# Performance work log

Measured on AMD Instinct MI355X. Metric: run time of the kernel, lower is better.

Reference implementation:

```python
import math
import jax
import jax.numpy as jnp
import numpy as np

B = 64          # graphs per batch
NPG = 1000      # nodes per graph
IN = 64         # input feature dim
H = 128         # hidden dim
DEG = 16        # avg degree
C = 10          # num classes
RATIO = 0.8     # topk ratio
EPS = 1e-5      # batchnorm eps
E = B * NPG * DEG


def setup_inputs() -> dict:
    key = jax.random.key(0)
    ks = jax.random.split(key, 16)
    x = jax.random.normal(ks[0], (B * NPG, IN), jnp.float32)
    # per-graph random edges, then offset to global node ids
    src = jax.random.randint(ks[1], (B, NPG * DEG), 0, NPG)
    dst = jax.random.randint(ks[2], (B, NPG * DEG), 0, NPG)
    off = (jnp.arange(B) * NPG)[:, None]
    edge_index = jnp.stack([(src + off).reshape(-1), (dst + off).reshape(-1)]).astype(jnp.int32)
    batch = jnp.repeat(jnp.arange(B), NPG).astype(jnp.int32)
    edge_weight = jax.random.uniform(ks[3], (E,), jnp.float32)
    # parameters: block 1 conv is [IN,H]; blocks 2-6 are [H,H] (stacked)
    conv1_w = jax.random.normal(ks[4], (IN, H), jnp.float32) * 0.05
    conv_w = jax.random.normal(ks[5], (5, H, H), jnp.float32) * 0.05
    conv_b = jnp.zeros((6, H), jnp.float32)
    bn_gamma = jnp.ones((6, H), jnp.float32)
    bn_beta = jnp.zeros((6, H), jnp.float32)
    bn_mean = jax.random.normal(ks[6], (6, H), jnp.float32) * 0.01
    bn_var = jax.random.uniform(ks[7], (6, H), jnp.float32, 0.5, 1.5)
    pool_w = jax.random.normal(ks[8], (6, H), jnp.float32)
    d1_w = jax.random.normal(ks[9], (2 * H, 4 * H), jnp.float32) * 0.05
    d1_b = jnp.zeros((4 * H,), jnp.float32)
    d2_w = jax.random.normal(ks[10], (4 * H, C), jnp.float32) * 0.05
    d2_b = jnp.zeros((C,), jnp.float32)
    return dict(x=x, edge_index=edge_index, batch=batch, edge_weight=edge_weight,
                conv1_w=conv1_w, conv_w=conv_w, conv_b=conv_b,
                bn_gamma=bn_gamma, bn_beta=bn_beta, bn_mean=bn_mean, bn_var=bn_var,
                pool_w=pool_w, d1_w=d1_w, d1_b=d1_b, d2_w=d2_w, d2_b=d2_b)


def _gcn_conv(h, src, dst, w_e, W, b, n_nodes):
    # PyG GCNConv: add self-loops (weight 1), sym-normalize, aggregate at dst
    xw = h @ W                                        # [N, H]
    deg = jnp.zeros((n_nodes,), h.dtype).at[dst].add(w_e) + 1.0
    dinv = jax.lax.rsqrt(deg)
    coef = dinv[src] * dinv[dst] * w_e                # [E]
    out = jnp.zeros_like(xw).at[dst].add(coef[:, None] * xw[src])
    out = out + (dinv * dinv)[:, None] * xw + b       # self-loop term + bias
    return out


def reference(x, edge_index, batch, edge_weight, conv1_w, conv_w, conv_b,
              bn_gamma, bn_beta, bn_mean, bn_var, pool_w, d1_w, d1_b, d2_w, d2_b):
    src, dst = edge_index[0], edge_index[1]
    w_e = edge_weight
    h = x
    n_cur = NPG
    flats = jnp.zeros((B, 2 * H), x.dtype)
    for i in range(6):
        N = B * n_cur
        W = conv1_w if i == 0 else conv_w[i - 1]
        hc = _gcn_conv(h, src, dst, w_e, W, conv_b[i], N)
        # BatchNorm (inference) + ReLU
        hc = (hc - bn_mean[i]) * (bn_gamma[i] * jax.lax.rsqrt(bn_var[i] + EPS)) + bn_beta[i]
        hc = jax.nn.relu(hc)
        # TopKPooling: score = tanh(x.w/||w||), keep top ceil(ratio*n) per graph
        pw = pool_w[i]
        score = jnp.tanh(hc @ pw / jnp.linalg.norm(pw))   # [N]
        k = math.ceil(RATIO * n_cur)
        vals, idx = jax.lax.top_k(score.reshape(B, n_cur), k)  # [B,k]
        perm = (idx + (jnp.arange(B) * n_cur)[:, None]).reshape(-1)
        h = hc[perm] * vals.reshape(-1, 1)                # [B*k, H]
        # remap/filter edges; dead edges become (0,0) with weight 0
        inv = jnp.full((N,), -1, jnp.int32).at[perm].set(jnp.arange(B * k, dtype=jnp.int32))
        ok = (inv[src] >= 0) & (inv[dst] >= 0)
        src = jnp.where(ok, inv[src], 0)
        dst = jnp.where(ok, inv[dst], 0)
        w_e = jnp.where(ok, w_e, 0.0)
        n_cur = k
        hb = h.reshape(B, k, H)
        flats = flats + jnp.concatenate([hb.mean(axis=1), hb.max(axis=1)], axis=-1)
    # MLP head (dropout is identity in eval)
    hd = jax.nn.relu(flats @ d1_w + d1_b)
    return hd @ d2_w + d2_b
```

## Files before the change

kernel.cpp:

```cpp
#include <hip/hip_runtime.h>
#include <float.h>
#include <math.h>

#define NGR 64
#define NPG0 1000
#define HDIM 128
#define EG 16000
#define NE (NGR*EG)
#define RPS 1008
#define BNEPS 1e-5f
#define POOL_NB 16

typedef short short8 __attribute__((ext_vector_type(8)));
typedef float f4v __attribute__((ext_vector_type(4)));

__global__ __launch_bounds__(256) void k_wsplit(const float* __restrict__ c1w,
    const float* __restrict__ cw, const float* __restrict__ pw,
    unsigned short* __restrict__ wh, unsigned short* __restrict__ wl,
    float* __restrict__ invnorm){
  int l = blockIdx.x, t = threadIdx.x;
  __shared__ float red[2];
  if(t < 128){
    float v = pw[l*HDIM + t];
    float s = v*v;
    #pragma unroll
    for(int o=32;o>0;o>>=1) s += __shfl_down(s, o, 64);
    if((t & 63)==0) red[t>>6] = s;
  }
  __syncthreads();
  if(t==0) invnorm[l] = 1.0f / sqrtf(red[0]+red[1]);
  int K  = (l==0) ? 64 : 128;
  int sh = (l==0) ? 6 : 7;
  const float* src = (l==0) ? c1w : (cw + (size_t)(l-1)*16384);
  int tot = 128*K;
  for(int o=t;o<tot;o+=256){
    int c = o >> sh, k = o & (K-1);
    float f = src[k*128 + c];
    unsigned u  = __float_as_uint(f);
    unsigned uh = (u + 0x7fffu + ((u>>16)&1u)) & 0xffff0000u;
    float r = f - __uint_as_float(uh);
    unsigned v = __float_as_uint(r);
    int o2 = (k>>3)*1024 + c*8 + (k&7);
    wh[(size_t)l*16384 + o2] = (unsigned short)(uh>>16);
    wl[(size_t)l*16384 + o2] = (unsigned short)((v + 0x7fffu + ((v>>16)&1u))>>16);
  }
}

__global__ __launch_bounds__(256) void k_count0(const int* __restrict__ dst,
    const float* __restrict__ we, int* __restrict__ pcnt, float* __restrict__ pdeg){
  int g = blockIdx.x >> 2, sub = blockIdx.x & 3, t = threadIdx.x;
  __shared__ int   cnt[NPG0];
  __shared__ float degl[NPG0];
  for(int i=t;i<NPG0;i+=256){ cnt[i]=0; degl[i]=0.f; }
  __syncthreads();
  int base = g*EG + sub*4000;
  for(int idx=t; idx<4000; idx+=256){
    int e = base + idx;
    int ld = dst[e] - g*NPG0;
    atomicAdd(&cnt[ld], 1);
    atomicAdd(&degl[ld], we[e]);
  }
  __syncthreads();
  int p = blockIdx.x * NPG0;
  for(int i=t;i<NPG0;i+=256){ pcnt[p+i] = cnt[i]; pdeg[p+i] = degl[i]; }
}

__global__ __launch_bounds__(1024) void k_build(const int* __restrict__ pcnt,
    const float* __restrict__ pdeg, const int* __restrict__ src,
    const int* __restrict__ dst, const float* __restrict__ we,
    int* __restrict__ rp, float* __restrict__ dinvz, float* __restrict__ gsc,
    long long* __restrict__ ec){
  int g = blockIdx.x, t = threadIdx.x;
  __shared__ int sc[2][1024];
  __shared__ int cur[NPG0];
  int c = 0;
  if(t < NPG0){
    c = pcnt[(g*4+0)*NPG0+t] + pcnt[(g*4+1)*NPG0+t]
      + pcnt[(g*4+2)*NPG0+t] + pcnt[(g*4+3)*NPG0+t];
    float dg = pdeg[(g*4+0)*NPG0+t] + pdeg[(g*4+1)*NPG0+t]
             + pdeg[(g*4+2)*NPG0+t] + pdeg[(g*4+3)*NPG0+t];
    float dv = 1.0f / sqrtf(dg + 1.0f);
    dinvz[g*NPG0+t] = dv;
    gsc[g*NPG0+t]   = dv;
  }
  sc[0][t] = c;
  __syncthreads();
  int buf = 0;
  for(int d=1; d<1024; d<<=1){
    int v = sc[buf][t];
    if(t>=d) v += sc[buf][t-d];
    sc[buf^1][t] = v;
    __syncthreads();
    buf ^= 1;
  }
  if(t<=NPG0) rp[g*RPS+t] = (t==0) ? 0 : sc[buf][t-1];
  if(t<NPG0)  cur[t]      = (t==0) ? 0 : sc[buf][t-1];
  __syncthreads();
  int base = g*EG;
  for(int idx=t; idx<EG; idx+=1024){
    int e = base + idx;
    int ld = dst[e] - g*NPG0;
    int pos = atomicAdd(&cur[ld], 1);
    ec[(size_t)base + pos] = (((long long)__float_as_int(we[e]))<<32) | (unsigned)src[e];
  }
}

template<int L0>
__global__ __launch_bounds__(256) void k_agg(int n, const int* __restrict__ nlist,
    const int* __restrict__ rp, const long long* __restrict__ ec,
    const float* __restrict__ dinvz, const float* __restrict__ gsc,
    const float* __restrict__ h, float* __restrict__ agg){
  int g = blockIdx.x & 63;
  int chunk = blockIdx.x >> 6;
  int wid = threadIdx.x >> 6, lane = threadIdx.x & 63;
  const int wpg = (gridDim.x >> 6) * 4;
  const int qw   = lane >> 4, sl16 = lane & 15;
  for(int j = chunk*4 + wid; j < n; j += wpg){
    int cg = g*n + j;
    int d  = L0 ? (g*NPG0 + j) : nlist[cg];
    int ld = d - g*NPG0;
    int e0 = rp[g*RPS+ld], e1 = rp[g*RPS+ld+1];
    float dvd = dinvz[d];
    float gsd = gsc[d];
    float4 a0; a0.x=0.f; a0.y=0.f; a0.z=0.f; a0.w=0.f;
    float4 a1; a1.x=0.f; a1.y=0.f; a1.z=0.f; a1.w=0.f;
    for(int b=e0;b<e1;b+=64){
      int mm = e1-b; if(mm>64) mm=64;
      long long rec = (lane<mm) ? ec[(size_t)g*EG + b + lane] : 0;
      int   sl = (int)(rec & 0xffffffffLL);
      float cl = __int_as_float((int)(rec>>32)) * gsc[sl];
      long long pk = (((long long)__float_as_int(cl))<<32) | (unsigned)sl;
      int mr = (mm+15) & ~15;
      for(int jj=0;jj<mr;jj+=16){
        #pragma unroll
        for(int u=0;u<4;u++){
          long long p = __shfl(pk, jj + 4*u + qw, 64);
          float c = __int_as_float((int)(p>>32));
          if(c != 0.f){
            int s = (int)(p & 0xffffffffLL);
            if(L0){
              float4 hv = *(const float4*)(h + (size_t)s*64 + 4*sl16);
              a0.x += c*hv.x; a0.y += c*hv.y; a0.z += c*hv.z; a0.w += c*hv.w;
            } else {
              const float4* hp = (const float4*)(h + (size_t)s*HDIM + 8*sl16);
              float4 h0 = hp[0], h1 = hp[1];
              a0.x += c*h0.x; a0.y += c*h0.y; a0.z += c*h0.z; a0.w += c*h0.w;
              a1.x += c*h1.x; a1.y += c*h1.y; a1.z += c*h1.z; a1.w += c*h1.w;
            }
          }
        }
      }
    }
    a0.x += __shfl_xor(a0.x, 16, 64); a0.y += __shfl_xor(a0.y, 16, 64);
    a0.z += __shfl_xor(a0.z, 16, 64); a0.w += __shfl_xor(a0.w, 16, 64);
    a0.x += __shfl_xor(a0.x, 32, 64); a0.y += __shfl_xor(a0.y, 32, 64);
    a0.z += __shfl_xor(a0.z, 32, 64); a0.w += __shfl_xor(a0.w, 32, 64);
    if(!L0){
      a1.x += __shfl_xor(a1.x, 16, 64); a1.y += __shfl_xor(a1.y, 16, 64);
      a1.z += __shfl_xor(a1.z, 16, 64); a1.w += __shfl_xor(a1.w, 16, 64);
      a1.x += __shfl_xor(a1.x, 32, 64); a1.y += __shfl_xor(a1.y, 32, 64);
      a1.z += __shfl_xor(a1.z, 32, 64); a1.w += __shfl_xor(a1.w, 32, 64);
    }
    if(qw==0){
      if(L0){
        float4 hs = *(const float4*)(h + (size_t)d*64 + 4*sl16);
        float4 o;
        o.x = dvd*(a0.x + gsd*hs.x); o.y = dvd*(a0.y + gsd*hs.y);
        o.z = dvd*(a0.z + gsd*hs.z); o.w = dvd*(a0.w + gsd*hs.w);
        *(float4*)(agg + (size_t)cg*64 + 4*sl16) = o;
      } else {
        const float4* hp = (const float4*)(h + (size_t)d*HDIM + 8*sl16);
        float4 s0 = hp[0], s1 = hp[1];
        float4 o0, o1;
        o0.x = dvd*(a0.x + gsd*s0.x); o0.y = dvd*(a0.y + gsd*s0.y);
        o0.z = dvd*(a0.z + gsd*s0.z); o0.w = dvd*(a0.w + gsd*s0.w);
        o1.x = dvd*(a1.x + gsd*s1.x); o1.y = dvd*(a1.y + gsd*s1.y);
        o1.z = dvd*(a1.z + gsd*s1.z); o1.w = dvd*(a1.w + gsd*s1.w);
        float4* op = (float4*)(agg + (size_t)cg*HDIM + 8*sl16);
        op[0] = o0; op[1] = o1;
      }
    }
  }
}

__device__ inline void bfsplit(float f, unsigned short &h, unsigned short &l){
  unsigned u  = __float_as_uint(f);
  unsigned uh = (u + 0x7fffu + ((u>>16)&1u)) & 0xffff0000u;
  float r = f - __uint_as_float(uh);
  unsigned v = __float_as_uint(r);
  h = (unsigned short)(uh>>16);
  l = (unsigned short)((v + 0x7fffu + ((v>>16)&1u))>>16);
}

template<int KIN>
__global__ __launch_bounds__(256) void k_gemm_mfma(const float* __restrict__ Ain,
    const unsigned short* __restrict__ Wh, const unsigned short* __restrict__ Wl,
    const float* __restrict__ bias, const float* __restrict__ gamma,
    const float* __restrict__ beta, const float* __restrict__ mean,
    const float* __restrict__ var, const float* __restrict__ pw,
    const float* __restrict__ invn_p, const int* __restrict__ olist,
    float* __restrict__ hout, float* __restrict__ score){
  __shared__ __attribute__((aligned(16))) unsigned short AsH[64*KIN];
  __shared__ __attribute__((aligned(16))) unsigned short AsL[64*KIN];
  __shared__ float sp[64][2];
  int t = threadIdx.x;
  int r0 = blockIdx.x * 64;
  const int lane = t & 63, wid = t >> 6;
  const int wr = wid >> 1, wc = wid & 1;
  const int lr = lane & 15, lq = lane >> 4;

  constexpr int ACH = KIN/4;
  constexpr int ANP = 64*ACH/256;
  #pragma unroll
  for(int p=0;p<ANP;p++){
    int idx = p*256 + t;
    int row = idx / ACH, cq = idx % ACH;
    float4 a = *(const float4*)(Ain + (size_t)(r0+row)*KIN + cq*4);
    ushort4 h4, l4;
    bfsplit(a.x, h4.x, l4.x); bfsplit(a.y, h4.y, l4.y);
    bfsplit(a.z, h4.z, l4.z); bfsplit(a.w, h4.w, l4.w);
    int off = (row*(KIN*2) + cq*8) ^ ((row&7)<<4);
    *(ushort4*)((char*)AsH + off) = h4;
    *(ushort4*)((char*)AsL + off) = l4;
  }
  __syncthreads();

  f4v acc[2][4];
  #pragma unroll
  for(int m=0;m<2;m++)
    #pragma unroll
    for(int n=0;n<4;n++){ acc[m][n][0]=0.f; acc[m][n][1]=0.f; acc[m][n][2]=0.f; acc[m][n][3]=0.f; }

  #pragma unroll
  for(int ks=0; ks<KIN/32; ks++){
    short8 ah[2], al[2], bh[4], bl[4];
    int kb = ks*64 + lq*16;
    int panel = ks*4 + lq;
    #pragma unroll
    for(int n=0;n<4;n++){
      int col = wc*64 + n*16 + lr;
      int goff = (panel*128 + col)*8;
      bh[n] = *(const short8*)(Wh + goff);
      bl[n] = *(const short8*)(Wl + goff);
    }
    #pragma unroll
    for(int m=0;m<2;m++){
      int row = wr*32 + m*16 + lr;
      int off = (row*(KIN*2) + kb) ^ ((row&7)<<4);
      ah[m] = *(const short8*)((const char*)AsH + off);
      al[m] = *(const short8*)((const char*)AsL + off);
    }
    #pragma unroll
    for(int m=0;m<2;m++){
      #pragma unroll
      for(int n=0;n<4;n++){
        acc[m][n] = __builtin_amdgcn_mfma_f32_16x16x32_bf16(ah[m], bh[n], acc[m][n], 0,0,0);
        acc[m][n] = __builtin_amdgcn_mfma_f32_16x16x32_bf16(ah[m], bl[n], acc[m][n], 0,0,0);
        acc[m][n] = __builtin_amdgcn_mfma_f32_16x16x32_bf16(al[m], bh[n], acc[m][n], 0,0,0);
        acc[m][n] = __builtin_amdgcn_mfma_f32_16x16x32_bf16(al[m], bl[n], acc[m][n], 0,0,0);
      }
    }
  }

  float invn = invn_p[0];
  float bi[4], scv[4], bt[4], mn[4], pv[4];
  #pragma unroll
  for(int n=0;n<4;n++){
    int c = wc*64 + n*16 + lr;
    bi[n]  = bias[c];
    scv[n] = gamma[c] * (1.0f/sqrtf(var[c] + BNEPS));
    bt[n]  = beta[c];
    mn[n]  = mean[c];
    pv[n]  = pw[c];
  }
  #pragma unroll
  for(int m=0;m<2;m++){
    #pragma unroll
    for(int i=0;i<4;i++){
      int rl  = wr*32 + m*16 + lq*4 + i;
      int row = r0 + rl;
      int orig = olist ? olist[row] : row;
      float p = 0.f;
      #pragma unroll
      for(int n=0;n<4;n++){
        float v = fmaxf((acc[m][n][i] + bi[n] - mn[n])*scv[n] + bt[n], 0.f);
        hout[(size_t)orig*HDIM + wc*64 + n*16 + lr] = v;
        p += v*pv[n];
      }
      p += __shfl_xor(p, 1, 64); p += __shfl_xor(p, 2, 64);
      p += __shfl_xor(p, 4, 64); p += __shfl_xor(p, 8, 64);
      if(lr==0) sp[rl][wc] = p;
    }
  }
  __syncthreads();
  if(t < 64) score[r0 + t] = tanhf((sp[t][0] + sp[t][1]) * invn);
}

__global__ __launch_bounds__(512) void k_topk(int n, int k,
    const float* __restrict__ score, const int* __restrict__ curlist,
    float* __restrict__ vals, int* __restrict__ nextlist,
    float* __restrict__ dinvz, float* __restrict__ gsc){
  int g = blockIdx.x, t = threadIdx.x;
  __shared__ unsigned keys[1024];
  __shared__ int hist[256];
  __shared__ int ssum[256];
  __shared__ int sc2[2][512];
  __shared__ int eqbuf[1024];
  __shared__ int eqn;
  __shared__ int sh_B, sh_need, sh_E, sh_cut;
  __shared__ unsigned sh_pref;
  for(int i=t;i<n;i+=512){
    unsigned b = __float_as_uint(score[g*n+i]);
    keys[i] = (b & 0x80000000u) ? ~b : (b | 0x80000000u);
  }
  if(t==0){ sh_need = k; sh_pref = 0u; sh_cut = 0x7fffffff; }
  __syncthreads();
  for(int pass=0; pass<4; pass++){
    int shift = 24 - 8*pass;
    if(t<256) hist[t]=0;
    __syncthreads();
    unsigned pref = sh_pref; int need = sh_need;
    for(int i=t;i<n;i+=512){
      unsigned u = keys[i];
      bool m = (pass==0) || ((u >> (shift+8)) == pref);
      if(m) atomicAdd(&hist[(u>>shift)&255], 1);
    }
    __syncthreads();
    if(t<256) ssum[t] = hist[t];
    __syncthreads();
    for(int d=1; d<256; d<<=1){
      int v=0;
      if(t<256) v = ssum[t] + ((t+d<256)? ssum[t+d] : 0);
      __syncthreads();
      if(t<256) ssum[t] = v;
      __syncthreads();
    }
    if(t<256){
      int Sgt = ssum[t] - hist[t];
      if(Sgt < need && need <= ssum[t]) sh_B = t;
    }
    __syncthreads();
    int B = sh_B;
    if(t==0){
      sh_need = need - (ssum[B] - hist[B]);
      sh_pref = (pass==0) ? (unsigned)B : ((pref<<8) | (unsigned)B);
      if(pass==3) sh_E = hist[B];
    }
    __syncthreads();
  }
  unsigned T = sh_pref; int r_eq = sh_need; int E = sh_E;
  if(E > r_eq){
    if(t==0) eqn = 0;
    __syncthreads();
    for(int i=t;i<n;i+=512) if(keys[i]==T){ int p=atomicAdd(&eqn,1); eqbuf[p]=i; }
    __syncthreads();
    if(t==0){
      int last = -1;
      for(int j=0;j<r_eq;j++){
        int mn = 0x7fffffff;
        for(int q=0;q<E;q++){ int v=eqbuf[q]; if(v>last && v<mn) mn=v; }
        last = mn;
      }
      sh_cut = last;
    }
    __syncthreads();
  }
  int cut = sh_cut;
  int c0=0, c1=0;
  {
    int i=t;
    if(i<n){ unsigned u=keys[i]; c0 = (u>T) || (u==T && i<=cut); }
    i=t+512;
    if(i<n){ unsigned u=keys[i]; c1 = (u>T) || (u==T && i<=cut); }
  }
  sc2[0][t] = c0+c1;
  __syncthreads();
  int buf=0;
  for(int d=1; d<512; d<<=1){
    int v = sc2[buf][t];
    if(t>=d) v += sc2[buf][t-d];
    sc2[buf^1][t]=v;
    __syncthreads();
    buf^=1;
  }
  int base = (t==0) ? 0 : sc2[buf][t-1];
  {
    int i=t;
    if(i<n){
      int orig = curlist ? curlist[g*n+i] : (g*NPG0 + i);
      if(c0){
        unsigned u=keys[i];
        float f = __uint_as_float((u & 0x80000000u) ? (u ^ 0x80000000u) : ~u);
        vals[g*k+base]=f; nextlist[g*k+base]=orig; base++;
      } else { dinvz[orig]=0.f; gsc[orig]=0.f; }
    }
    i=t+512;
    if(i<n){
      int orig = curlist ? curlist[g*n+i] : (g*NPG0 + i);
      if(c1){
        unsigned u=keys[i];
        float f = __uint_as_float((u & 0x80000000u) ? (u ^ 0x80000000u) : ~u);
        vals[g*k+base]=f; nextlist[g*k+base]=orig;
      } else { dinvz[orig]=0.f; gsc[orig]=0.f; }
    }
  }
}

__global__ __launch_bounds__(256) void k_gpd(int k, int do_deg,
    const float* __restrict__ hraw, const float* __restrict__ vals,
    const int* __restrict__ nextlist,
    float* __restrict__ sumst, float* __restrict__ maxst,
    const int* __restrict__ rp, const long long* __restrict__ ec,
    float* __restrict__ dinvz, float* __restrict__ gsc){
  int g = blockIdx.x & 63;
  int chunk = blockIdx.x >> 6;
  int wid = threadIdx.x >> 6, lane = threadIdx.x & 63;
  int ww = chunk*4 + wid;
  const int half = lane >> 5, sl32 = lane & 31;
  const int qw   = lane >> 4, sl16 = lane & 15;
  const int NH = POOL_NB*4*2;
  float4 psum; psum.x=0.f; psum.y=0.f; psum.z=0.f; psum.w=0.f;
  float4 pmax; pmax.x=-FLT_MAX; pmax.y=-FLT_MAX; pmax.z=-FLT_MAX; pmax.w=-FLT_MAX;
  for(int j = ww*2 + half; j < k; j += NH){
    float v = vals[g*k+j];
    int d = nextlist[g*k+j];
    float4 hv = *(const float4*)(hraw + (size_t)d*HDIM + 4*sl32);
    float4 o; o.x=hv.x*v; o.y=hv.y*v; o.z=hv.z*v; o.w=hv.w*v;
    psum.x+=o.x; psum.y+=o.y; psum.z+=o.z; psum.w+=o.w;
    pmax.x=fmaxf(pmax.x,o.x); pmax.y=fmaxf(pmax.y,o.y);
    pmax.z=fmaxf(pmax.z,o.z); pmax.w=fmaxf(pmax.w,o.w);
  }
  if(do_deg){
    const int NQ = POOL_NB*4*4;
    for(int j = ww*4 + qw; j < k; j += NQ){
      int d  = nextlist[g*k + j];
      int ld = d - g*NPG0;
      int e0 = rp[g*RPS+ld], e1 = rp[g*RPS+ld+1];
      float deg = 0.f;
      for(int b=e0+sl16; b<e1; b+=16){
        long long rec = ec[(size_t)g*EG + b];
        int s = (int)(rec & 0xffffffffLL);
        float w = __int_as_float((int)(rec>>32));
        if(dinvz[s] != 0.f) deg += w;
      }
      #pragma unroll
      for(int o=8;o>0;o>>=1) deg += __shfl_xor(deg, o, 64);
      if(sl16==0){
        float dv = 1.0f / sqrtf(deg + 1.0f);
        dinvz[d] = dv;
        gsc[d] = dv * vals[g*k+j];
      }
    }
  }
  psum.x += __shfl_xor(psum.x, 32, 64); psum.y += __shfl_xor(psum.y, 32, 64);
  psum.z += __shfl_xor(psum.z, 32, 64); psum.w += __shfl_xor(psum.w, 32, 64);
  pmax.x = fmaxf(pmax.x, __shfl_xor(pmax.x, 32, 64));
  pmax.y = fmaxf(pmax.y, __shfl_xor(pmax.y, 32, 64));
  pmax.z = fmaxf(pmax.z, __shfl_xor(pmax.z, 32, 64));
  pmax.w = fmaxf(pmax.w, __shfl_xor(pmax.w, 32, 64));
  __shared__ float ss[4][128];
  __shared__ float sm[4][128];
  if(half==0){
    *(float4*)&ss[wid][4*sl32] = psum;
    *(float4*)&sm[wid][4*sl32] = pmax;
  }
  __syncthreads();
  int t = threadIdx.x;
  if(t < 128){
    float s = (ss[0][t]+ss[1][t]) + (ss[2][t]+ss[3][t]);
    float m = fmaxf(fmaxf(sm[0][t], sm[1][t]), fmaxf(sm[2][t], sm[3][t]));
    sumst[(size_t)(chunk*NGR + g)*HDIM + t] = s;
    maxst[(size_t)(chunk*NGR + g)*HDIM + t] = m;
  }
}

__global__ __launch_bounds__(512) void k_head(const float* __restrict__ sumstage,
    const float* __restrict__ maxstage,
    const float* __restrict__ d1w, const float* __restrict__ d1b,
    const float* __restrict__ d2w, const float* __restrict__ d2b, float* __restrict__ out){
  const float kinv[6] = {1.f/800.f, 1.f/640.f, 1.f/512.f, 1.f/410.f, 1.f/328.f, 1.f/263.f};
  int g = blockIdx.x, j = threadIdx.x;
  __shared__ float fl[256];
  __shared__ float hd[512];
  if(j < 128){
    float s = 0.f;
    #pragma unroll
    for(int l=0;l<6;l++){
      float ls = 0.f;
      for(int c=0;c<POOL_NB;c++)
        ls += sumstage[(size_t)((l*POOL_NB + c)*NGR + g)*HDIM + j];
      s += ls * kinv[l];
    }
    fl[j] = s;
  } else if(j < 256){
    int f = j - 128;
    float m = 0.f;
    #pragma unroll
    for(int l=0;l<6;l++){
      float lm = -FLT_MAX;
      for(int c=0;c<POOL_NB;c++)
        lm = fmaxf(lm, maxstage[(size_t)((l*POOL_NB + c)*NGR + g)*HDIM + f]);
      m += lm;
    }
    fl[j] = m;
  }
  __syncthreads();
  float acc = d1b[j];
  for(int i=0;i<256;i++) acc += fl[i]*d1w[i*512+j];
  hd[j] = fmaxf(acc, 0.f);
  __syncthreads();
  if(j < 10){
    float a = d2b[j];
    for(int i=0;i<512;i++) a += hd[i]*d2w[i*10+j];
    out[g*10+j] = a;
  }
}

extern "C" void kernel_launch(void* const* d_in, const int* in_sizes, int n_in,
                              void* d_out, int out_size, void* d_ws, size_t ws_size,
                              hipStream_t stream) {
  const float* x    = (const float*)d_in[0];
  const int* ei     = (const int*)d_in[1];
  const float* ew   = (const float*)d_in[3];
  const float* conv1w = (const float*)d_in[4];
  const float* convw  = (const float*)d_in[5];
  const float* convb  = (const float*)d_in[6];
  const float* bng    = (const float*)d_in[7];
  const float* bnb    = (const float*)d_in[8];
  const float* bnm    = (const float*)d_in[9];
  const float* bnv    = (const float*)d_in[10];
  const float* poolw  = (const float*)d_in[11];
  const float* d1w    = (const float*)d_in[12];
  const float* d1b    = (const float*)d_in[13];
  const float* d2w    = (const float*)d_in[14];
  const float* d2b    = (const float*)d_in[15];
  float* out = (float*)d_out;

  char* w = (char*)d_ws;
  float* horig = (float*)w; w += (size_t)64000*128*4;
  float* hc    = (float*)w; w += (size_t)64000*128*4;
  float* agg0  = (float*)w; w += (size_t)64000*64*4;
  long long* ec = (long long*)w; w += (size_t)NE*8;
  int*   rp    = (int*)w;   w += (size_t)NGR*RPS*4;
  int*   pcnt  = (int*)w;   w += (size_t)256*NPG0*4;
  float* pdeg  = (float*)w; w += (size_t)256*NPG0*4;
  float* dinvz = (float*)w; w += (size_t)64000*4;
  float* gsc   = (float*)w; w += (size_t)64000*4;
  float* score = (float*)w; w += (size_t)64000*4;
  float* vals  = (float*)w; w += (size_t)51200*4;
  int*   listA = (int*)w;   w += (size_t)51200*4;
  int*   listB = (int*)w;   w += (size_t)51200*4;
  float* invno = (float*)w; w += 64;
  float* sumstage = (float*)w; w += (size_t)6*POOL_NB*NGR*HDIM*4;
  float* maxstage = (float*)w; w += (size_t)6*POOL_NB*NGR*HDIM*4;
  unsigned short* whi = (unsigned short*)w; w += (size_t)6*16384*2;
  unsigned short* wlo = (unsigned short*)w; w += (size_t)6*16384*2;

  k_wsplit<<<6,256,0,stream>>>(conv1w, convw, poolw, whi, wlo, invno);

  const int ns[6]={1000,800,640,512,410,328};
  const int ks[6]={800,640,512,410,328,263};

  k_count0<<<256,256,0,stream>>>(ei+NE, ew, pcnt, pdeg);
  k_build<<<64,1024,0,stream>>>(pcnt, pdeg, ei, ei+NE, ew, rp, dinvz, gsc, ec);

  k_agg<1><<<64*32,256,0,stream>>>(1000, nullptr, rp, ec, dinvz, gsc, x, agg0);
  k_gemm_mfma<64><<<1000,256,0,stream>>>(agg0, whi, wlo, convb, bng, bnb, bnm, bnv,
                                         poolw, invno, nullptr, horig, score);
  k_topk<<<64,512,0,stream>>>(1000, 800, score, nullptr, vals, listA, dinvz, gsc);
  k_gpd<<<64*POOL_NB,256,0,stream>>>(800, 1, horig, vals, listA,
                                     sumstage, maxstage, rp, ec, dinvz, gsc);

  int* cur = listA; int* nxt = listB;
  for(int i=1;i<6;i++){
    int n = ns[i], k = ks[i];
    k_agg<0><<<64*32,256,0,stream>>>(n, cur, rp, ec, dinvz, gsc, horig, hc);
    k_gemm_mfma<128><<<n,256,0,stream>>>(hc, whi + (size_t)i*16384, wlo + (size_t)i*16384,
                                         convb+i*128, bng+i*128, bnb+i*128, bnm+i*128,
                                         bnv+i*128, poolw+i*128, invno+i,
                                         cur, horig, score);
    k_topk<<<64,512,0,stream>>>(n, k, score, cur, vals, nxt, dinvz, gsc);
    k_gpd<<<64*POOL_NB,256,0,stream>>>(k, (i<5)?1:0, horig, vals, nxt,
                                       sumstage + (size_t)i*POOL_NB*NGR*HDIM,
                                       maxstage + (size_t)i*POOL_NB*NGR*HDIM,
                                       rp, ec, dinvz, gsc);
    int* tmp = cur; cur = nxt; nxt = tmp;
  }

  k_head<<<64,512,0,stream>>>(sumstage, maxstage, d1w, d1b, d2w, d2b, out);
}
```

Baseline: 484.4 us.

## Fuse neighbor aggregation into MFMA GEMM kernel via shared-memory tiles

Merges the per-layer aggregation kernel and the split-bf16 MFMA GEMM into one kernel. Each 256-thread block aggregates 32 rows (8 per wave) straight into swizzled hi/lo bf16 shared-memory tiles, then runs the GEMM, BN, ReLU and score epilogue. This drops the global round trip of the aggregated features and one launch per layer. Because the kernel now reads old h while writing new rows by original index, it ping-pongs between two h buffers. The cost is a smaller GEMM tile (32 rows, one m-fragment per wave) with less weight reuse, and a different aggregation parallel layout.

```diff
diff --git a/kernel.cpp b/kernel.cpp
--- a/kernel.cpp
+++ b/kernel.cpp
@@ -105,19 +105,41 @@
   }
 }
 
-template<int L0>
-__global__ __launch_bounds__(256) void k_agg(int n, const int* __restrict__ nlist,
+__device__ inline void bfsplit(float f, unsigned short &h, unsigned short &l){
+  unsigned u  = __float_as_uint(f);
+  unsigned uh = (u + 0x7fffu + ((u>>16)&1u)) & 0xffff0000u;
+  float r = f - __uint_as_float(uh);
+  unsigned v = __float_as_uint(r);
+  h = (unsigned short)(uh>>16);
+  l = (unsigned short)((v + 0x7fffu + ((v>>16)&1u))>>16);
+}
+
+template<int KIN>
+__global__ __launch_bounds__(256) void k_fused(const int* __restrict__ olist,
     const int* __restrict__ rp, const long long* __restrict__ ec,
     const float* __restrict__ dinvz, const float* __restrict__ gsc,
-    const float* __restrict__ h, float* __restrict__ agg){
-  int g = blockIdx.x & 63;
-  int chunk = blockIdx.x >> 6;
-  int wid = threadIdx.x >> 6, lane = threadIdx.x & 63;
-  const int wpg = (gridDim.x >> 6) * 4;
-  const int qw   = lane >> 4, sl16 = lane & 15;
-  for(int j = chunk*4 + wid; j < n; j += wpg){
-    int cg = g*n + j;
-    int d  = L0 ? (g*NPG0 + j) : nlist[cg];
+    const float* __restrict__ h,
+    const unsigned short* __restrict__ Wh, const unsigned short* __restrict__ Wl,
+    const float* __restrict__ bias, const float* __restrict__ gamma,
+    const float* __restrict__ beta, const float* __restrict__ mean,
+    const float* __restrict__ var, const float* __restrict__ pw,
+    const float* __restrict__ invn_p, float* __restrict__ hout,
+    float* __restrict__ score){
+  constexpr int L0 = (KIN==64);
+  __shared__ __attribute__((aligned(16))) unsigned short AsH[32*KIN];
+  __shared__ __attribute__((aligned(16))) unsigned short AsL[32*KIN];
+  __shared__ float sp[32][2];
+  int t = threadIdx.x;
+  int r0 = blockIdx.x * 32;
+  const int lane = t & 63, wid = t >> 6;
+  const int wr = wid >> 1, wc = wid & 1;
+  const int qw = lane >> 4, sl16 = lane & 15;
+
+  for(int rr=0; rr<8; rr++){
+    int local = wid*8 + rr;
+    int row = r0 + local;
+    int d = L0 ? row : olist[row];
+    int g = d / NPG0;
     int ld = d - g*NPG0;
     int e0 = rp[g*RPS+ld], e1 = rp[g*RPS+ld+1];
     float dvd = dinvz[d];
@@ -167,7 +189,12 @@
         float4 o;
         o.x = dvd*(a0.x + gsd*hs.x); o.y = dvd*(a0.y + gsd*hs.y);
         o.z = dvd*(a0.z + gsd*hs.z); o.w = dvd*(a0.w + gsd*hs.w);
-        *(float4*)(agg + (size_t)cg*64 + 4*sl16) = o;
+        ushort4 h4, l4;
+        bfsplit(o.x, h4.x, l4.x); bfsplit(o.y, h4.y, l4.y);
+        bfsplit(o.z, h4.z, l4.z); bfsplit(o.w, h4.w, l4.w);
+        int off = (local*128 + sl16*8) ^ ((local&7)<<4);
+        *(ushort4*)((char*)AsH + off) = h4;
+        *(ushort4*)((char*)AsL + off) = l4;
       } else {
         const float4* hp = (const float4*)(h + (size_t)d*HDIM + 8*sl16);
         float4 s0 = hp[0], s1 = hp[1];
@@ -176,89 +203,48 @@
         o0.z = dvd*(a0.z + gsd*s0.z); o0.w = dvd*(a0.w + gsd*s0.w);
         o1.x = dvd*(a1.x + gsd*s1.x); o1.y = dvd*(a1.y + gsd*s1.y);
         o1.z = dvd*(a1.z + gsd*s1.z); o1.w = dvd*(a1.w + gsd*s1.w);
-        float4* op = (float4*)(agg + (size_t)cg*HDIM + 8*sl16);
-        op[0] = o0; op[1] = o1;
+        ushort4 h4, l4;
+        int off = (local*256 + sl16*16) ^ ((local&7)<<4);
+        bfsplit(o0.x, h4.x, l4.x); bfsplit(o0.y, h4.y, l4.y);
+        bfsplit(o0.z, h4.z, l4.z); bfsplit(o0.w, h4.w, l4.w);
+        *(ushort4*)((char*)AsH + off) = h4;
+        *(ushort4*)((char*)AsL + off) = l4;
+        bfsplit(o1.x, h4.x, l4.x); bfsplit(o1.y, h4.y, l4.y);
+        bfsplit(o1.z, h4.z, l4.z); bfsplit(o1.w, h4.w, l4.w);
+        *(ushort4*)((char*)AsH + off + 8) = h4;
+        *(ushort4*)((char*)AsL + off + 8) = l4;
       }
     }
   }
-}
-
-__device__ inline void bfsplit(float f, unsigned short &h, unsigned short &l){
-  unsigned u  = __float_as_uint(f);
-  unsigned uh = (u + 0x7fffu + ((u>>16)&1u)) & 0xffff0000u;
-  float r = f - __uint_as_float(uh);
-  unsigned v = __float_as_uint(r);
-  h = (unsigned short)(uh>>16);
-  l = (unsigned short)((v + 0x7fffu + ((v>>16)&1u))>>16);
-}
-
-template<int KIN>
-__global__ __launch_bounds__(256) void k_gemm_mfma(const float* __restrict__ Ain,
-    const unsigned short* __restrict__ Wh, const unsigned short* __restrict__ Wl,
-    const float* __restrict__ bias, const float* __restrict__ gamma,
-    const float* __restrict__ beta, const float* __restrict__ mean,
-    const float* __restrict__ var, const float* __restrict__ pw,
-    const float* __restrict__ invn_p, const int* __restrict__ olist,
-    float* __restrict__ hout, float* __restrict__ score){
-  __shared__ __attribute__((aligned(16))) unsigned short AsH[64*KIN];
-  __shared__ __attribute__((aligned(16))) unsigned short AsL[64*KIN];
-  __shared__ float sp[64][2];
-  int t = threadIdx.x;
-  int r0 = blockIdx.x * 64;
-  const int lane = t & 63, wid = t >> 6;
-  const int wr = wid >> 1, wc = wid & 1;
-  const int lr = lane & 15, lq = lane >> 4;
-
-  constexpr int ACH = KIN/4;
-  constexpr int ANP = 64*ACH/256;
+  __syncthreads();
+
+  f4v acc[4];
   #pragma unroll
-  for(int p=0;p<ANP;p++){
-    int idx = p*256 + t;
-    int row = idx / ACH, cq = idx % ACH;
-    float4 a = *(const float4*)(Ain + (size_t)(r0+row)*KIN + cq*4);
-    ushort4 h4, l4;
-    bfsplit(a.x, h4.x, l4.x); bfsplit(a.y, h4.y, l4.y);
-    bfsplit(a.z, h4.z, l4.z); bfsplit(a.w, h4.w, l4.w);
-    int off = (row*(KIN*2) + cq*8) ^ ((row&7)<<4);
-    *(ushort4*)((char*)AsH + off) = h4;
-    *(ushort4*)((char*)AsL + off) = l4;
-  }
-  __syncthreads();
-
-  f4v acc[2][4];
-  #pragma unroll
-  for(int m=0;m<2;m++)
-    #pragma unroll
-    for(int n=0;n<4;n++){ acc[m][n][0]=0.f; acc[m][n][1]=0.f; acc[m][n][2]=0.f; acc[m][n][3]=0.f; }
-
+  for(int n=0;n<4;n++){ acc[n][0]=0.f; acc[n][1]=0.f; acc[n][2]=0.f; acc[n][3]=0.f; }
   #pragma unroll
   for(int ks=0; ks<KIN/32; ks++){
-    short8 ah[2], al[2], bh[4], bl[4];
-    int kb = ks*64 + lq*16;
-    int panel = ks*4 + lq;
+    short8 ah, al, bh[4], bl[4];
+    int kb = ks*64 + qw*16;
+    int panel = ks*4 + qw;
     #pragma unroll
     for(int n=0;n<4;n++){
-      int col = wc*64 + n*16 + lr;
+      int col = wc*64 + n*16 + sl16;
       int goff = (panel*128 + col)*8;
       bh[n] = *(const short8*)(Wh + goff);
       bl[n] = *(const short8*)(Wl + goff);
     }
+    {
+      int row = wr*16 + sl16;
+      int off = (row*(KIN*2) + kb) ^ ((row&7)<<4);
+      ah = *(const short8*)((const char*)AsH + off);
+      al = *(const short8*)((const char*)AsL + off);
+    }
     #pragma unroll
-    for(int m=0;m<2;m++){
-      int row = wr*32 + m*16 + lr;
-      int off = (row*(KIN*2) + kb) ^ ((row&7)<<4);
-      ah[m] = *(const short8*)((const char*)AsH + off);
-      al[m] = *(const short8*)((const char*)AsL + off);
-    }
-    #pragma unroll
-    for(int m=0;m<2;m++){
-      #pragma unroll
-      for(int n=0;n<4;n++){
-        acc[m][n] = __builtin_amdgcn_mfma_f32_16x16x32_bf16(ah[m], bh[n], acc[m][n], 0,0,0);
-        acc[m][n] = __builtin_amdgcn_mfma_f32_16x16x32_bf16(ah[m], bl[n], acc[m][n], 0,0,0);
-        acc[m][n] = __builtin_amdgcn_mfma_f32_16x16x32_bf16(al[m], bh[n], acc[m][n], 0,0,0);
-        acc[m][n] = __builtin_amdgcn_mfma_f32_16x16x32_bf16(al[m], bl[n], acc[m][n], 0,0,0);
-      }
+    for(int n=0;n<4;n++){
+      acc[n] = __builtin_amdgcn_mfma_f32_16x16x32_bf16(ah, bh[n], acc[n], 0,0,0);
+      acc[n] = __builtin_amdgcn_mfma_f32_16x16x32_bf16(ah, bl[n], acc[n], 0,0,0);
+      acc[n] = __builtin_amdgcn_mfma_f32_16x16x32_bf16(al, bh[n], acc[n], 0,0,0);
+      acc[n] = __builtin_amdgcn_mfma_f32_16x16x32_bf16(al, bl[n], acc[n], 0,0,0);
     }
   }
 
@@ -266,7 +252,7 @@
   float bi[4], scv[4], bt[4], mn[4], pv[4];
   #pragma unroll
   for(int n=0;n<4;n++){
-    int c = wc*64 + n*16 + lr;
+    int c = wc*64 + n*16 + sl16;
     bi[n]  = bias[c];
     scv[n] = gamma[c] * (1.0f/sqrtf(var[c] + BNEPS));
     bt[n]  = beta[c];
@@ -274,26 +260,23 @@
     pv[n]  = pw[c];
   }
   #pragma unroll
-  for(int m=0;m<2;m++){
+  for(int i=0;i<4;i++){
+    int rl  = wr*16 + qw*4 + i;
+    int row = r0 + rl;
+    int orig = olist ? olist[row] : row;
+    float p = 0.f;
     #pragma unroll
-    for(int i=0;i<4;i++){
-      int rl  = wr*32 + m*16 + lq*4 + i;
-      int row = r0 + rl;
-      int orig = olist ? olist[row] : row;
-      float p = 0.f;
-      #pragma unroll
-      for(int n=0;n<4;n++){
-        float v = fmaxf((acc[m][n][i] + bi[n] - mn[n])*scv[n] + bt[n], 0.f);
-        hout[(size_t)orig*HDIM + wc*64 + n*16 + lr] = v;
-        p += v*pv[n];
-      }
-      p += __shfl_xor(p, 1, 64); p += __shfl_xor(p, 2, 64);
-      p += __shfl_xor(p, 4, 64); p += __shfl_xor(p, 8, 64);
-      if(lr==0) sp[rl][wc] = p;
-    }
-  }
-  __syncthreads();
-  if(t < 64) score[r0 + t] = tanhf((sp[t][0] + sp[t][1]) * invn);
+    for(int n=0;n<4;n++){
+      float v = fmaxf((acc[n][i] + bi[n] - mn[n])*scv[n] + bt[n], 0.f);
+      hout[(size_t)orig*HDIM + wc*64 + n*16 + sl16] = v;
+      p += v*pv[n];
+    }
+    p += __shfl_xor(p, 1, 64); p += __shfl_xor(p, 2, 64);
+    p += __shfl_xor(p, 4, 64); p += __shfl_xor(p, 8, 64);
+    if(sl16==0) sp[rl][wc] = p;
+  }
+  __syncthreads();
+  if(t < 32) score[r0 + t] = tanhf((sp[t][0] + sp[t][1]) * invn);
 }
 
 __global__ __launch_bounds__(512) void k_topk(int n, int k,
@@ -537,9 +520,8 @@
   float* out = (float*)d_out;
 
   char* w = (char*)d_ws;
-  float* horig = (float*)w; w += (size_t)64000*128*4;
-  float* hc    = (float*)w; w += (size_t)64000*128*4;
-  float* agg0  = (float*)w; w += (size_t)64000*64*4;
+  float* hbufA = (float*)w; w += (size_t)64000*128*4;
+  float* hbufB = (float*)w; w += (size_t)64000*128*4;
   long long* ec = (long long*)w; w += (size_t)NE*8;
   int*   rp    = (int*)w;   w += (size_t)NGR*RPS*4;
   int*   pcnt  = (int*)w;   w += (size_t)256*NPG0*4;
@@ -564,27 +546,29 @@
   k_count0<<<256,256,0,stream>>>(ei+NE, ew, pcnt, pdeg);
   k_build<<<64,1024,0,stream>>>(pcnt, pdeg, ei, ei+NE, ew, rp, dinvz, gsc, ec);
 
-  k_agg<1><<<64*32,256,0,stream>>>(1000, nullptr, rp, ec, dinvz, gsc, x, agg0);
-  k_gemm_mfma<64><<<1000,256,0,stream>>>(agg0, whi, wlo, convb, bng, bnb, bnm, bnv,
-                                         poolw, invno, nullptr, horig, score);
+  k_fused<64><<<2000,256,0,stream>>>(nullptr, rp, ec, dinvz, gsc, x, whi, wlo,
+                                     convb, bng, bnb, bnm, bnv, poolw, invno,
+                                     hbufA, score);
   k_topk<<<64,512,0,stream>>>(1000, 800, score, nullptr, vals, listA, dinvz, gsc);
-  k_gpd<<<64*POOL_NB,256,0,stream>>>(800, 1, horig, vals, listA,
+  k_gpd<<<64*POOL_NB,256,0,stream>>>(800, 1, hbufA, vals, listA,
                                      sumstage, maxstage, rp, ec, dinvz, gsc);
 
   int* cur = listA; int* nxt = listB;
+  float* hin = hbufA; float* hot = hbufB;
   for(int i=1;i<6;i++){
     int n = ns[i], k = ks[i];
-    k_agg<0><<<64*32,256,0,stream>>>(n, cur, rp, ec, dinvz, gsc, horig, hc);
-    k_gemm_mfma<128><<<n,256,0,stream>>>(hc, whi + (size_t)i*16384, wlo + (size_t)i*16384,
-                                         convb+i*128, bng+i*128, bnb+i*128, bnm+i*128,
-                                         bnv+i*128, poolw+i*128, invno+i,
-                                         cur, horig, score);
+    k_fused<128><<<2*n,256,0,stream>>>(cur, rp, ec, dinvz, gsc, hin,
+                                       whi + (size_t)i*16384, wlo + (size_t)i*16384,
+                                       convb+i*128, bng+i*128, bnb+i*128, bnm+i*128,
+                                       bnv+i*128, poolw+i*128, invno+i,
+                                       hot, score);
     k_topk<<<64,512,0,stream>>>(n, k, score, cur, vals, nxt, dinvz, gsc);
-    k_gpd<<<64*POOL_NB,256,0,stream>>>(k, (i<5)?1:0, horig, vals, nxt,
+    k_gpd<<<64*POOL_NB,256,0,stream>>>(k, (i<5)?1:0, hot, vals, nxt,
                                        sumstage + (size_t)i*POOL_NB*NGR*HDIM,
                                        maxstage + (size_t)i*POOL_NB*NGR*HDIM,
                                        rp, ec, dinvz, gsc);
     int* tmp = cur; cur = nxt; nxt = tmp;
+    float* htmp = hin; hin = hot; hot = htmp;
   }
 
   k_head<<<64,512,0,stream>>>(sumstage, maxstage, d1w, d1b, d2w, d2b, out);
```

Result: slower. 575.3 us (+18.8%).
